# Kernel tuning notes

Hardware: AMD Instinct MI355X
Metric: run time of the kernel (lower is better)

## Reference

```python
import jax, jax.numpy as jnp
import numpy as np

N_NODES = 50000
ELU_ALPHA = 0.2  # torch.nn.ELU(0.2): alpha=0.2


def _elu(v, alpha):
    return jnp.where(v > 0, v, alpha * jnp.expm1(v))


def setup_inputs() -> dict:
    key = jax.random.key(0)
    k1, k2, k3, k4, k5 = jax.random.split(key, 5)
    fin, H, F = 128, 4, 32
    E = 1600000
    return {
        "x": jax.random.normal(k1, (N_NODES, fin), dtype=jnp.float32),
        "W": jax.random.normal(k2, (fin, H * F), dtype=jnp.float32) * (1.414 / np.sqrt(fin)),
        "a_src": jax.random.normal(k3, (H, F), dtype=jnp.float32) * 0.1,
        "a_tgt": jax.random.normal(k4, (H, F), dtype=jnp.float32) * 0.1,
        "edge_index": jax.random.randint(k5, (E, 2), 0, N_NODES, dtype=jnp.int64),
    }


def reference(x, W, a_src, a_tgt, edge_index):
    # GAT layer (dropout omitted: eval mode). x: [N, fin]
    N = x.shape[0]
    H, F = a_src.shape
    xp = (x @ W).reshape(N, H, F)                 # projected node feats [N,H,F]
    s_src = jnp.einsum("nhf,hf->nh", xp, a_src)   # per-head source scores [N,H]
    s_tgt = jnp.einsum("nhf,hf->nh", xp, a_tgt)   # per-head target scores [N,H]

    src = edge_index[:, 0]
    tgt = edge_index[:, 1]

    # edge-wise gather (the memory-bound hotspot)
    e = _elu(s_src[src] + s_tgt[tgt], ELU_ALPHA)  # [E,H]

    # segment softmax over edges sharing a target node
    m = jax.ops.segment_max(e, tgt, num_segments=N)           # [N,H]
    m = jnp.where(jnp.isfinite(m), m, 0.0)
    ex = jnp.exp(e - m[tgt])                                  # [E,H]
    denom = jax.ops.segment_sum(ex, tgt, num_segments=N)      # [N,H]
    alpha = ex / denom[tgt]                                   # [E,H]

    # gather source features, weight, scatter-add into target nodes
    msg = alpha[:, :, None] * xp[src]                          # [E,H,F]
    out = jax.ops.segment_sum(msg, tgt, num_segments=N)        # [N,H,F]
    return out.reshape(N, H * F)                               # concat heads
```

## Files before the change

### kernel.cpp

```cpp
#include <hip/hip_runtime.h>
#include <hip/hip_bf16.h>
#include <math.h>

#define FIN 128
#define NHEAD 4
#define CH 128
#define ELU_A 0.2f

#define BSHIFT 8
#define NB 196
#define CAP 16384
#define T_EDGES 2048

typedef unsigned int uint32;
typedef __attribute__((ext_vector_type(8))) short short8;
typedef __attribute__((ext_vector_type(4))) float f32x4;

__device__ __forceinline__ float bf16lo(uint32 u) {
    union { uint32 i; float f; } c; c.i = u << 16; return c.f;
}
__device__ __forceinline__ float bf16hi(uint32 u) {
    union { uint32 i; float f; } c; c.i = u & 0xffff0000u; return c.f;
}
__device__ __forceinline__ unsigned short f2b(float f) {
    union { float f; uint32 u; } c; c.f = f;
    uint32 u = c.u;
    return (unsigned short)((u + 0x7fffu + ((u >> 16) & 1u)) >> 16);
}

union SMem {
    struct {
        uint32 stage[T_EDGES];
        int hist[256], scanbuf[256], loff[256], cnt2[256], base[256];
    } p;
    unsigned short wt[128][136];
    unsigned short cbuf[4][16][132];
};

__global__ __launch_bounds__(256) void mega_kernel(
    const int2* __restrict__ ei2, int* __restrict__ bcnt,
    uint32* __restrict__ ebuck, const float* __restrict__ x,
    const float* __restrict__ W, unsigned short* __restrict__ xpb,
    const float* __restrict__ a_src, const float* __restrict__ a_tgt,
    float* __restrict__ s_src, float* __restrict__ s_tgt,
    int E, int N, int PB)
{
    __shared__ SMem sm;
    const int tid = threadIdx.x;

    if ((int)blockIdx.x < PB) {
        const int e0 = blockIdx.x * T_EDGES;
        const int tile = min(T_EDGES, E - e0);

        sm.p.hist[tid] = 0; sm.p.cnt2[tid] = 0;
        __syncthreads();

        uint32 rec[8];
#pragma unroll
        for (int j = 0; j < 8; ++j) {
            int idx = e0 + j * 256 + tid;
            if (idx < E) {
                int2 p = ei2[idx];
                rec[j] = (uint32)p.x | ((uint32)p.y << 16);
                atomicAdd(&sm.p.hist[p.y >> BSHIFT], 1);
            } else rec[j] = 0xFFFFFFFFu;
        }
        __syncthreads();

        sm.p.scanbuf[tid] = sm.p.hist[tid];
        __syncthreads();
        for (int off = 1; off < 256; off <<= 1) {
            int v = (tid >= off) ? sm.p.scanbuf[tid - off] : 0;
            __syncthreads();
            sm.p.scanbuf[tid] += v;
            __syncthreads();
        }
        sm.p.loff[tid] = sm.p.scanbuf[tid] - sm.p.hist[tid];
        if (tid < NB && sm.p.hist[tid] > 0)
            sm.p.base[tid] = tid * CAP + atomicAdd(&bcnt[tid], sm.p.hist[tid]);
        __syncthreads();

#pragma unroll
        for (int j = 0; j < 8; ++j) {
            if (rec[j] != 0xFFFFFFFFu) {
                int b = rec[j] >> (16 + BSHIFT);
                int r = atomicAdd(&sm.p.cnt2[b], 1);
                sm.p.stage[sm.p.loff[b] + r] = rec[j];
            }
        }
        __syncthreads();

        for (int i = tid; i < tile; i += 256) {
            uint32 rc = sm.p.stage[i];
            int b = rc >> (16 + BSHIFT);
            ebuck[(size_t)sm.p.base[b] + (i - sm.p.loff[b])] = rc;
        }
        return;
    }

    const int gb = blockIdx.x - PB;

    for (int i = tid; i < FIN * CH / 2; i += 256) {
        int n  = i & 127;
        int k2 = i >> 7;
        float w0 = W[(size_t)(2 * k2 + 0) * CH + n];
        float w1 = W[(size_t)(2 * k2 + 1) * CH + n];
        uint32 pk = (uint32)f2b(w0) | ((uint32)f2b(w1) << 16);
        *(uint32*)&sm.wt[n][2 * k2] = pk;
    }
    __syncthreads();

    const int lane = tid & 63;
    const int wid  = tid >> 6;
    const int rowbase = gb * 64 + wid * 16;

    const int rr   = min(rowbase + (lane & 15), N - 1);
    const int krow = (lane >> 4) * 8;

    f32x4 acc[8];
#pragma unroll
    for (int c = 0; c < 8; ++c) acc[c] = (f32x4){0.f, 0.f, 0.f, 0.f};

#pragma unroll
    for (int s = 0; s < 4; ++s) {
        const int koff = s * 32 + krow;
        const float* xr = x + (size_t)rr * FIN + koff;
        float4 p0 = *(const float4*)xr;
        float4 p1 = *(const float4*)(xr + 4);
        short8 af;
        af[0] = (short)f2b(p0.x); af[1] = (short)f2b(p0.y);
        af[2] = (short)f2b(p0.z); af[3] = (short)f2b(p0.w);
        af[4] = (short)f2b(p1.x); af[5] = (short)f2b(p1.y);
        af[6] = (short)f2b(p1.z); af[7] = (short)f2b(p1.w);
#pragma unroll
        for (int c = 0; c < 8; ++c) {
            const short8 bf = *(const short8*)&sm.wt[c * 16 + (lane & 15)][koff];
            acc[c] = __builtin_amdgcn_mfma_f32_16x16x32_bf16(af, bf, acc[c], 0, 0, 0);
        }
    }
    __syncthreads();

#pragma unroll
    for (int c = 0; c < 8; ++c)
#pragma unroll
        for (int r = 0; r < 4; ++r)
            sm.cbuf[wid][(lane >> 4) * 4 + r][c * 16 + (lane & 15)] = f2b(acc[c][r]);
    __syncthreads();

    for (int r = 0; r < 16; ++r) {
        int row = rowbase + r;
        if (row < N) {
            uint32 v = *(const uint32*)&sm.cbuf[wid][r][lane * 2];
            *(uint32*)&xpb[(size_t)row * CH + lane * 2] = v;
        }
    }

    {
        const int srow = lane >> 2;
        const int sh   = lane & 3;
        const unsigned short* cp = &sm.cbuf[wid][srow][sh * 32];
        const float* as = a_src + sh * 32;
        const float* at = a_tgt + sh * 32;
        float ps = 0.f, pt = 0.f;
#pragma unroll
        for (int q = 0; q < 4; ++q) {
            uint4 u = *(const uint4*)&cp[q * 8];
            float4 a0 = *(const float4*)&as[q * 8];
            float4 a1 = *(const float4*)&as[q * 8 + 4];
            float4 b0 = *(const float4*)&at[q * 8];
            float4 b1 = *(const float4*)&at[q * 8 + 4];
            float l0 = bf16lo(u.x), h0 = bf16hi(u.x);
            float l1 = bf16lo(u.y), h1 = bf16hi(u.y);
            float l2 = bf16lo(u.z), h2 = bf16hi(u.z);
            float l3 = bf16lo(u.w), h3 = bf16hi(u.w);
            ps += l0*a0.x + h0*a0.y + l1*a0.z + h1*a0.w
                + l2*a1.x + h2*a1.y + l3*a1.z + h3*a1.w;
            pt += l0*b0.x + h0*b0.y + l1*b0.z + h1*b0.w
                + l2*b1.x + h2*b1.y + l3*b1.z + h3*b1.w;
        }
        int node = rowbase + srow;
        if (node < N) {
            s_src[(size_t)node * NHEAD + sh] = ps;
            s_tgt[(size_t)node * NHEAD + sh] = pt;
        }
    }
}

__global__ __launch_bounds__(1024) void fine_scatter_kernel(
    const uint32* __restrict__ ebuck, const int* __restrict__ bcnt,
    int* __restrict__ deg, int* __restrict__ rowptr,
    int* __restrict__ srcs, int N)
{
    __shared__ int ldeg[256], psum[256], lcur[256], red[256];
    const int b = blockIdx.x;
    const int tid = threadIdx.x;

    if (tid < 256) {
        red[tid]  = (tid < b) ? bcnt[tid] : 0;
        ldeg[tid] = 0;
    }
    __syncthreads();
    for (int off = 128; off >= 1; off >>= 1) {
        if (tid < off) red[tid] += red[tid + off];
        __syncthreads();
    }
    const int gb = red[0];

    const int cnt = bcnt[b];
    const uint32* rp = ebuck + (size_t)b * CAP;

    for (int i = tid; i < cnt; i += 1024)
        atomicAdd(&ldeg[(rp[i] >> 16) & 255], 1);
    __syncthreads();

    if (tid < 256) psum[tid] = ldeg[tid];
    __syncthreads();
    for (int off = 1; off < 256; off <<= 1) {
        int u = 0;
        if (tid < 256 && tid >= off) u = psum[tid - off];
        __syncthreads();
        if (tid < 256) psum[tid] += u;
        __syncthreads();
    }

    if (tid < 256) {
        int pref = gb + psum[tid] - ldeg[tid];
        lcur[tid] = pref;
        int node = b * 256 + tid;
        if (node < N) { deg[node] = ldeg[tid]; rowptr[node] = pref; }
    }
    __syncthreads();

    for (int i = tid; i < cnt; i += 1024) {
        uint32 rc = rp[i];
        int pos = atomicAdd(&lcur[(rc >> 16) & 255], 1);
        srcs[pos] = rc & 0xffff;
    }
}

__global__ __launch_bounds__(256) void aggregate_kernel(
    const int* __restrict__ srcs, const int* __restrict__ rowptr,
    const int* __restrict__ deg, const float* __restrict__ s_src,
    const float* __restrict__ s_tgt, const uint32* __restrict__ xpb,
    float* __restrict__ out, int N)
{
    const int lane = threadIdx.x & 63;
    const int wid  = __builtin_amdgcn_readfirstlane(threadIdx.x >> 6);
    const int t = blockIdx.x * 4 + wid;
    if (t >= N) return;

    const int start = __builtin_amdgcn_readfirstlane(rowptr[t]);
    const int d     = __builtin_amdgcn_readfirstlane(deg[t]);
    const int h     = lane >> 4;
    const float st_h = s_tgt[(size_t)t * NHEAD + h];

    float accx = 0.0f, accy = 0.0f, dsum = 0.0f;
    int k = 0;

#define ACC(E, X) { dsum += (E); accx += (E) * bf16lo(X); accy += (E) * bf16hi(X); }

    const int cj16 = lane & 15;
    const int bb16 = h * 16;
    for (; k + 16 <= d; k += 16) {
        int   sv = srcs[start + k + cj16];
        float a  = s_src[(size_t)sv * NHEAD + h];
        float v  = a + st_h;
        float u  = v > 0.0f ? v : ELU_A * (__expf(v) - 1.0f);
        float e  = __expf(u);

        int s0 = srcs[start + k + 0],  s1 = srcs[start + k + 1];
        int s2 = srcs[start + k + 2],  s3 = srcs[start + k + 3];
        int s4 = srcs[start + k + 4],  s5 = srcs[start + k + 5];
        int s6 = srcs[start + k + 6],  s7 = srcs[start + k + 7];
        int s8 = srcs[start + k + 8],  s9 = srcs[start + k + 9];
        int sa = srcs[start + k + 10], sb = srcs[start + k + 11];
        int sc = srcs[start + k + 12], sd = srcs[start + k + 13];
        int se = srcs[start + k + 14], sf = srcs[start + k + 15];

        uint32 x0 = xpb[(size_t)s0 * 64 + lane], x1 = xpb[(size_t)s1 * 64 + lane];
        uint32 x2 = xpb[(size_t)s2 * 64 + lane], x3 = xpb[(size_t)s3 * 64 + lane];
        uint32 x4 = xpb[(size_t)s4 * 64 + lane], x5 = xpb[(size_t)s5 * 64 + lane];
        uint32 x6 = xpb[(size_t)s6 * 64 + lane], x7 = xpb[(size_t)s7 * 64 + lane];
        uint32 x8 = xpb[(size_t)s8 * 64 + lane], x9 = xpb[(size_t)s9 * 64 + lane];
        uint32 xa = xpb[(size_t)sa * 64 + lane], xb = xpb[(size_t)sb * 64 + lane];
        uint32 xc = xpb[(size_t)sc * 64 + lane], xd = xpb[(size_t)sd * 64 + lane];
        uint32 xe = xpb[(size_t)se * 64 + lane], xf = xpb[(size_t)sf * 64 + lane];

        float e0 = __shfl(e, bb16 + 0),  e1 = __shfl(e, bb16 + 1);
        float e2 = __shfl(e, bb16 + 2),  e3 = __shfl(e, bb16 + 3);
        float e4 = __shfl(e, bb16 + 4),  e5 = __shfl(e, bb16 + 5);
        float e6 = __shfl(e, bb16 + 6),  e7 = __shfl(e, bb16 + 7);
        float e8 = __shfl(e, bb16 + 8),  e9 = __shfl(e, bb16 + 9);
        float ea = __shfl(e, bb16 + 10), eb = __shfl(e, bb16 + 11);
        float ec = __shfl(e, bb16 + 12), ed = __shfl(e, bb16 + 13);
        float ee = __shfl(e, bb16 + 14), ef = __shfl(e, bb16 + 15);

        ACC(e0, x0) ACC(e1, x1) ACC(e2, x2) ACC(e3, x3)
        ACC(e4, x4) ACC(e5, x5) ACC(e6, x6) ACC(e7, x7)
        ACC(e8, x8) ACC(e9, x9) ACC(ea, xa) ACC(eb, xb)
        ACC(ec, xc) ACC(ed, xd) ACC(ee, xe) ACC(ef, xf)
    }

    const int cj8 = lane & 7;
    const int chh = (lane >> 3) & 3;
    const float st_c = s_tgt[(size_t)t * NHEAD + chh];
    const int bb8 = h * 8;
    for (; k + 8 <= d; k += 8) {
        int   sv = srcs[start + k + cj8];
        float a  = s_src[(size_t)sv * NHEAD + chh];
        float v  = a + st_c;
        float u  = v > 0.0f ? v : ELU_A * (__expf(v) - 1.0f);
        float e  = __expf(u);

        int s0 = srcs[start + k + 0], s1 = srcs[start + k + 1];
        int s2 = srcs[start + k + 2], s3 = srcs[start + k + 3];
        int s4 = srcs[start + k + 4], s5 = srcs[start + k + 5];
        int s6 = srcs[start + k + 6], s7 = srcs[start + k + 7];

        uint32 x0 = xpb[(size_t)s0 * 64 + lane], x1 = xpb[(size_t)s1 * 64 + lane];
        uint32 x2 = xpb[(size_t)s2 * 64 + lane], x3 = xpb[(size_t)s3 * 64 + lane];
        uint32 x4 = xpb[(size_t)s4 * 64 + lane], x5 = xpb[(size_t)s5 * 64 + lane];
        uint32 x6 = xpb[(size_t)s6 * 64 + lane], x7 = xpb[(size_t)s7 * 64 + lane];

        float e0 = __shfl(e, bb8 + 0), e1 = __shfl(e, bb8 + 1);
        float e2 = __shfl(e, bb8 + 2), e3 = __shfl(e, bb8 + 3);
        float e4 = __shfl(e, bb8 + 4), e5 = __shfl(e, bb8 + 5);
        float e6 = __shfl(e, bb8 + 6), e7 = __shfl(e, bb8 + 7);

        ACC(e0, x0) ACC(e1, x1) ACC(e2, x2) ACC(e3, x3)
        ACC(e4, x4) ACC(e5, x5) ACC(e6, x6) ACC(e7, x7)
    }

    for (; k < d; ++k) {
        int   s  = srcs[start + k];
        float a  = s_src[(size_t)s * NHEAD + h];
        uint32 xv = xpb[(size_t)s * 64 + lane];
        float v = a + st_h;
        float u = v > 0.0f ? v : ELU_A * (__expf(v) - 1.0f);
        float e = __expf(u);
        ACC(e, xv)
    }
#undef ACC

    float inv = (d > 0) ? 1.0f / dsum : 0.0f;
    float2 o = make_float2(accx * inv, accy * inv);
    *(float2*)&out[(size_t)t * CH + lane * 2] = o;
}

extern "C" void kernel_launch(void* const* d_in, const int* in_sizes, int n_in,
                              void* d_out, int out_size, void* d_ws, size_t ws_size,
                              hipStream_t stream)
{
    const float* x     = (const float*)d_in[0];
    const float* W     = (const float*)d_in[1];
    const float* a_src = (const float*)d_in[2];
    const float* a_tgt = (const float*)d_in[3];
    const int*   ei    = (const int*)d_in[4];

    const int N = in_sizes[0] / FIN;
    const int E = in_sizes[4] / 2;
    const int PB = (E + T_EDGES - 1) / T_EDGES;
    const int GB = (N + 63) / 64;

    char* ws = (char*)d_ws;
    unsigned short* xpb = (unsigned short*)ws;  ws += (size_t)N * CH * sizeof(unsigned short);
    float* s_src  = (float*)ws;                 ws += (size_t)N * NHEAD * sizeof(float);
    float* s_tgt  = (float*)ws;                 ws += (size_t)N * NHEAD * sizeof(float);
    int*   deg    = (int*)ws;                   ws += (size_t)N * sizeof(int);
    int*   bcnt   = (int*)ws;                   ws += (size_t)NB * sizeof(int);
    int*   rowptr = (int*)ws;                   ws += (size_t)N * sizeof(int);
    int*   srcs   = (int*)ws;                   ws += (size_t)E * sizeof(int);
    uint32* ebuck = (uint32*)ws;                ws += (size_t)NB * CAP * sizeof(uint32);

    float* out = (float*)d_out;
    const int2* ei2 = (const int2*)ei;

    hipMemsetAsync(bcnt, 0, (size_t)NB * sizeof(int), stream);

    mega_kernel<<<PB + GB, 256, 0, stream>>>(
        ei2, bcnt, ebuck, x, W, xpb, a_src, a_tgt, s_src, s_tgt, E, N, PB);
    fine_scatter_kernel<<<NB, 1024, 0, stream>>>(
        ebuck, bcnt, deg, rowptr, srcs, N);
    aggregate_kernel<<<(N + 3) / 4, 256, 0, stream>>>(
        srcs, rowptr, deg, s_src, s_tgt, (const uint32*)xpb, out, N);
}
```

Before: 120.5 us.

## Fuse fine scatter into aggregation with per-block CSR held in LDS

Merges the fine-scatter and aggregate kernels into one. Each of four blocks per coarse bucket rescans the bucket, builds degree and prefix for its 64 nodes, and places source indices in shared memory; its waves then aggregate 8 nodes each. This removes the global deg/rowptr/srcs round trip and one launch. In exchange each bucket is read four times, each wave walks its nodes serially with fewer waves in flight, and a fixed LDS capacity silently drops edges when a 64-node group has too many.

After: 142.7 us. 18.4% more time.

```diff
diff --git a/kernel.cpp b/kernel.cpp
--- a/kernel.cpp
+++ b/kernel.cpp
@@ -11,6 +11,7 @@
 #define NB 196
 #define CAP 16384
 #define T_EDGES 2048
+#define LCAP 2944
 
 typedef unsigned int uint32;
 typedef __attribute__((ext_vector_type(8))) short short8;
@@ -186,165 +187,158 @@
     }
 }
 
-__global__ __launch_bounds__(1024) void fine_scatter_kernel(
+__global__ __launch_bounds__(512) void scatter_aggregate_kernel(
     const uint32* __restrict__ ebuck, const int* __restrict__ bcnt,
-    int* __restrict__ deg, int* __restrict__ rowptr,
-    int* __restrict__ srcs, int N)
+    const float* __restrict__ s_src, const float* __restrict__ s_tgt,
+    const uint32* __restrict__ xpb, float* __restrict__ out, int N)
 {
-    __shared__ int ldeg[256], psum[256], lcur[256], red[256];
-    const int b = blockIdx.x;
+    __shared__ int lsrcs[LCAP];
+    __shared__ int ldeg[64], psum[64], lcur[64];
+    const int B   = blockIdx.x >> 2;
+    const int q   = blockIdx.x & 3;
     const int tid = threadIdx.x;
-
-    if (tid < 256) {
-        red[tid]  = (tid < b) ? bcnt[tid] : 0;
-        ldeg[tid] = 0;
-    }
-    __syncthreads();
-    for (int off = 128; off >= 1; off >>= 1) {
-        if (tid < off) red[tid] += red[tid + off];
-        __syncthreads();
-    }
-    const int gb = red[0];
-
-    const int cnt = bcnt[b];
-    const uint32* rp = ebuck + (size_t)b * CAP;
-
-    for (int i = tid; i < cnt; i += 1024)
-        atomicAdd(&ldeg[(rp[i] >> 16) & 255], 1);
-    __syncthreads();
-
-    if (tid < 256) psum[tid] = ldeg[tid];
-    __syncthreads();
-    for (int off = 1; off < 256; off <<= 1) {
+    const int node0 = B * 256 + q * 64;
+
+    if (tid < 64) ldeg[tid] = 0;
+    __syncthreads();
+
+    const int cnt = bcnt[B];
+    const uint32* rp = ebuck + (size_t)B * CAP;
+
+    for (int i = tid; i < cnt; i += 512) {
+        uint32 rc = rp[i];
+        int local = (rc >> 16) & 255;
+        if ((local >> 6) == q) atomicAdd(&ldeg[local & 63], 1);
+    }
+    __syncthreads();
+
+    if (tid < 64) psum[tid] = ldeg[tid];
+    __syncthreads();
+    for (int off = 1; off < 64; off <<= 1) {
         int u = 0;
-        if (tid < 256 && tid >= off) u = psum[tid - off];
-        __syncthreads();
-        if (tid < 256) psum[tid] += u;
-        __syncthreads();
-    }
-
-    if (tid < 256) {
-        int pref = gb + psum[tid] - ldeg[tid];
-        lcur[tid] = pref;
-        int node = b * 256 + tid;
-        if (node < N) { deg[node] = ldeg[tid]; rowptr[node] = pref; }
-    }
-    __syncthreads();
-
-    for (int i = tid; i < cnt; i += 1024) {
+        if (tid < 64 && tid >= off) u = psum[tid - off];
+        __syncthreads();
+        if (tid < 64) psum[tid] += u;
+        __syncthreads();
+    }
+    if (tid < 64) lcur[tid] = psum[tid] - ldeg[tid];
+    __syncthreads();
+
+    for (int i = tid; i < cnt; i += 512) {
         uint32 rc = rp[i];
-        int pos = atomicAdd(&lcur[(rc >> 16) & 255], 1);
-        srcs[pos] = rc & 0xffff;
-    }
-}
-
-__global__ __launch_bounds__(256) void aggregate_kernel(
-    const int* __restrict__ srcs, const int* __restrict__ rowptr,
-    const int* __restrict__ deg, const float* __restrict__ s_src,
-    const float* __restrict__ s_tgt, const uint32* __restrict__ xpb,
-    float* __restrict__ out, int N)
-{
-    const int lane = threadIdx.x & 63;
-    const int wid  = __builtin_amdgcn_readfirstlane(threadIdx.x >> 6);
-    const int t = blockIdx.x * 4 + wid;
-    if (t >= N) return;
-
-    const int start = __builtin_amdgcn_readfirstlane(rowptr[t]);
-    const int d     = __builtin_amdgcn_readfirstlane(deg[t]);
-    const int h     = lane >> 4;
-    const float st_h = s_tgt[(size_t)t * NHEAD + h];
-
-    float accx = 0.0f, accy = 0.0f, dsum = 0.0f;
-    int k = 0;
+        int local = (rc >> 16) & 255;
+        if ((local >> 6) == q) {
+            int pos = atomicAdd(&lcur[local & 63], 1);
+            if (pos < LCAP) lsrcs[pos] = (int)(rc & 0xffff);
+        }
+    }
+    __syncthreads();
+
+    const int lane = tid & 63;
+    const int wid  = tid >> 6;
+    const int h    = lane >> 4;
 
 #define ACC(E, X) { dsum += (E); accx += (E) * bf16lo(X); accy += (E) * bf16hi(X); }
 
-    const int cj16 = lane & 15;
-    const int bb16 = h * 16;
-    for (; k + 16 <= d; k += 16) {
-        int   sv = srcs[start + k + cj16];
-        float a  = s_src[(size_t)sv * NHEAD + h];
-        float v  = a + st_h;
-        float u  = v > 0.0f ? v : ELU_A * (__expf(v) - 1.0f);
-        float e  = __expf(u);
-
-        int s0 = srcs[start + k + 0],  s1 = srcs[start + k + 1];
-        int s2 = srcs[start + k + 2],  s3 = srcs[start + k + 3];
-        int s4 = srcs[start + k + 4],  s5 = srcs[start + k + 5];
-        int s6 = srcs[start + k + 6],  s7 = srcs[start + k + 7];
-        int s8 = srcs[start + k + 8],  s9 = srcs[start + k + 9];
-        int sa = srcs[start + k + 10], sb = srcs[start + k + 11];
-        int sc = srcs[start + k + 12], sd = srcs[start + k + 13];
-        int se = srcs[start + k + 14], sf = srcs[start + k + 15];
-
-        uint32 x0 = xpb[(size_t)s0 * 64 + lane], x1 = xpb[(size_t)s1 * 64 + lane];
-        uint32 x2 = xpb[(size_t)s2 * 64 + lane], x3 = xpb[(size_t)s3 * 64 + lane];
-        uint32 x4 = xpb[(size_t)s4 * 64 + lane], x5 = xpb[(size_t)s5 * 64 + lane];
-        uint32 x6 = xpb[(size_t)s6 * 64 + lane], x7 = xpb[(size_t)s7 * 64 + lane];
-        uint32 x8 = xpb[(size_t)s8 * 64 + lane], x9 = xpb[(size_t)s9 * 64 + lane];
-        uint32 xa = xpb[(size_t)sa * 64 + lane], xb = xpb[(size_t)sb * 64 + lane];
-        uint32 xc = xpb[(size_t)sc * 64 + lane], xd = xpb[(size_t)sd * 64 + lane];
-        uint32 xe = xpb[(size_t)se * 64 + lane], xf = xpb[(size_t)sf * 64 + lane];
-
-        float e0 = __shfl(e, bb16 + 0),  e1 = __shfl(e, bb16 + 1);
-        float e2 = __shfl(e, bb16 + 2),  e3 = __shfl(e, bb16 + 3);
-        float e4 = __shfl(e, bb16 + 4),  e5 = __shfl(e, bb16 + 5);
-        float e6 = __shfl(e, bb16 + 6),  e7 = __shfl(e, bb16 + 7);
-        float e8 = __shfl(e, bb16 + 8),  e9 = __shfl(e, bb16 + 9);
-        float ea = __shfl(e, bb16 + 10), eb = __shfl(e, bb16 + 11);
-        float ec = __shfl(e, bb16 + 12), ed = __shfl(e, bb16 + 13);
-        float ee = __shfl(e, bb16 + 14), ef = __shfl(e, bb16 + 15);
-
-        ACC(e0, x0) ACC(e1, x1) ACC(e2, x2) ACC(e3, x3)
-        ACC(e4, x4) ACC(e5, x5) ACC(e6, x6) ACC(e7, x7)
-        ACC(e8, x8) ACC(e9, x9) ACC(ea, xa) ACC(eb, xb)
-        ACC(ec, xc) ACC(ed, xd) ACC(ee, xe) ACC(ef, xf)
-    }
-
-    const int cj8 = lane & 7;
-    const int chh = (lane >> 3) & 3;
-    const float st_c = s_tgt[(size_t)t * NHEAD + chh];
-    const int bb8 = h * 8;
-    for (; k + 8 <= d; k += 8) {
-        int   sv = srcs[start + k + cj8];
-        float a  = s_src[(size_t)sv * NHEAD + chh];
-        float v  = a + st_c;
-        float u  = v > 0.0f ? v : ELU_A * (__expf(v) - 1.0f);
-        float e  = __expf(u);
-
-        int s0 = srcs[start + k + 0], s1 = srcs[start + k + 1];
-        int s2 = srcs[start + k + 2], s3 = srcs[start + k + 3];
-        int s4 = srcs[start + k + 4], s5 = srcs[start + k + 5];
-        int s6 = srcs[start + k + 6], s7 = srcs[start + k + 7];
-
-        uint32 x0 = xpb[(size_t)s0 * 64 + lane], x1 = xpb[(size_t)s1 * 64 + lane];
-        uint32 x2 = xpb[(size_t)s2 * 64 + lane], x3 = xpb[(size_t)s3 * 64 + lane];
-        uint32 x4 = xpb[(size_t)s4 * 64 + lane], x5 = xpb[(size_t)s5 * 64 + lane];
-        uint32 x6 = xpb[(size_t)s6 * 64 + lane], x7 = xpb[(size_t)s7 * 64 + lane];
-
-        float e0 = __shfl(e, bb8 + 0), e1 = __shfl(e, bb8 + 1);
-        float e2 = __shfl(e, bb8 + 2), e3 = __shfl(e, bb8 + 3);
-        float e4 = __shfl(e, bb8 + 4), e5 = __shfl(e, bb8 + 5);
-        float e6 = __shfl(e, bb8 + 6), e7 = __shfl(e, bb8 + 7);
-
-        ACC(e0, x0) ACC(e1, x1) ACC(e2, x2) ACC(e3, x3)
-        ACC(e4, x4) ACC(e5, x5) ACC(e6, x6) ACC(e7, x7)
-    }
-
-    for (; k < d; ++k) {
-        int   s  = srcs[start + k];
-        float a  = s_src[(size_t)s * NHEAD + h];
-        uint32 xv = xpb[(size_t)s * 64 + lane];
-        float v = a + st_h;
-        float u = v > 0.0f ? v : ELU_A * (__expf(v) - 1.0f);
-        float e = __expf(u);
-        ACC(e, xv)
+    for (int i = 0; i < 8; ++i) {
+        const int ln = wid * 8 + i;
+        const int t  = node0 + ln;
+        if (t >= N) continue;
+
+        const int d     = ldeg[ln];
+        const int start = psum[ln] - d;
+        const float st_h = s_tgt[(size_t)t * NHEAD + h];
+
+        float accx = 0.0f, accy = 0.0f, dsum = 0.0f;
+        int k = 0;
+
+        const int cj16 = lane & 15;
+        const int bb16 = h * 16;
+        for (; k + 16 <= d; k += 16) {
+            int   sv = lsrcs[start + k + cj16];
+            float a  = s_src[(size_t)sv * NHEAD + h];
+            float v  = a + st_h;
+            float u  = v > 0.0f ? v : ELU_A * (__expf(v) - 1.0f);
+            float e  = __expf(u);
+
+            int s0 = lsrcs[start + k + 0],  s1 = lsrcs[start + k + 1];
+            int s2 = lsrcs[start + k + 2],  s3 = lsrcs[start + k + 3];
+            int s4 = lsrcs[start + k + 4],  s5 = lsrcs[start + k + 5];
+            int s6 = lsrcs[start + k + 6],  s7 = lsrcs[start + k + 7];
+            int s8 = lsrcs[start + k + 8],  s9 = lsrcs[start + k + 9];
+            int sa = lsrcs[start + k + 10], sb = lsrcs[start + k + 11];
+            int sc = lsrcs[start + k + 12], sd = lsrcs[start + k + 13];
+            int se = lsrcs[start + k + 14], sf = lsrcs[start + k + 15];
+
+            uint32 x0 = xpb[(size_t)s0 * 64 + lane], x1 = xpb[(size_t)s1 * 64 + lane];
+            uint32 x2 = xpb[(size_t)s2 * 64 + lane], x3 = xpb[(size_t)s3 * 64 + lane];
+            uint32 x4 = xpb[(size_t)s4 * 64 + lane], x5 = xpb[(size_t)s5 * 64 + lane];
+            uint32 x6 = xpb[(size_t)s6 * 64 + lane], x7 = xpb[(size_t)s7 * 64 + lane];
+            uint32 x8 = xpb[(size_t)s8 * 64 + lane], x9 = xpb[(size_t)s9 * 64 + lane];
+            uint32 xa = xpb[(size_t)sa * 64 + lane], xb = xpb[(size_t)sb * 64 + lane];
+            uint32 xc = xpb[(size_t)sc * 64 + lane], xd = xpb[(size_t)sd * 64 + lane];
+            uint32 xe = xpb[(size_t)se * 64 + lane], xf = xpb[(size_t)sf * 64 + lane];
+
+            float e0 = __shfl(e, bb16 + 0),  e1 = __shfl(e, bb16 + 1);
+            float e2 = __shfl(e, bb16 + 2),  e3 = __shfl(e, bb16 + 3);
+            float e4 = __shfl(e, bb16 + 4),  e5 = __shfl(e, bb16 + 5);
+            float e6 = __shfl(e, bb16 + 6),  e7 = __shfl(e, bb16 + 7);
+            float e8 = __shfl(e, bb16 + 8),  e9 = __shfl(e, bb16 + 9);
+            float ea = __shfl(e, bb16 + 10), eb = __shfl(e, bb16 + 11);
+            float ec = __shfl(e, bb16 + 12), ed = __shfl(e, bb16 + 13);
+            float ee = __shfl(e, bb16 + 14), ef = __shfl(e, bb16 + 15);
+
+            ACC(e0, x0) ACC(e1, x1) ACC(e2, x2) ACC(e3, x3)
+            ACC(e4, x4) ACC(e5, x5) ACC(e6, x6) ACC(e7, x7)
+            ACC(e8, x8) ACC(e9, x9) ACC(ea, xa) ACC(eb, xb)
+            ACC(ec, xc) ACC(ed, xd) ACC(ee, xe) ACC(ef, xf)
+        }
+
+        const int cj8 = lane & 7;
+        const int chh = (lane >> 3) & 3;
+        const float st_c = s_tgt[(size_t)t * NHEAD + chh];
+        const int bb8 = h * 8;
+        for (; k + 8 <= d; k += 8) {
+            int   sv = lsrcs[start + k + cj8];
+            float a  = s_src[(size_t)sv * NHEAD + chh];
+            float v  = a + st_c;
+            float u  = v > 0.0f ? v : ELU_A * (__expf(v) - 1.0f);
+            float e  = __expf(u);
+
+            int s0 = lsrcs[start + k + 0], s1 = lsrcs[start + k + 1];
+            int s2 = lsrcs[start + k + 2], s3 = lsrcs[start + k + 3];
+            int s4 = lsrcs[start + k + 4], s5 = lsrcs[start + k + 5];
+            int s6 = lsrcs[start + k + 6], s7 = lsrcs[start + k + 7];
+
+            uint32 x0 = xpb[(size_t)s0 * 64 + lane], x1 = xpb[(size_t)s1 * 64 + lane];
+            uint32 x2 = xpb[(size_t)s2 * 64 + lane], x3 = xpb[(size_t)s3 * 64 + lane];
+            uint32 x4 = xpb[(size_t)s4 * 64 + lane], x5 = xpb[(size_t)s5 * 64 + lane];
+            uint32 x6 = xpb[(size_t)s6 * 64 + lane], x7 = xpb[(size_t)s7 * 64 + lane];
+
+            float e0 = __shfl(e, bb8 + 0), e1 = __shfl(e, bb8 + 1);
+            float e2 = __shfl(e, bb8 + 2), e3 = __shfl(e, bb8 + 3);
+            float e4 = __shfl(e, bb8 + 4), e5 = __shfl(e, bb8 + 5);
+            float e6 = __shfl(e, bb8 + 6), e7 = __shfl(e, bb8 + 7);
+
+            ACC(e0, x0) ACC(e1, x1) ACC(e2, x2) ACC(e3, x3)
+            ACC(e4, x4) ACC(e5, x5) ACC(e6, x6) ACC(e7, x7)
+        }
+
+        for (; k < d; ++k) {
+            int   s  = lsrcs[start + k];
+            float a  = s_src[(size_t)s * NHEAD + h];
+            uint32 xv = xpb[(size_t)s * 64 + lane];
+            float v = a + st_h;
+            float u = v > 0.0f ? v : ELU_A * (__expf(v) - 1.0f);
+            float e = __expf(u);
+            ACC(e, xv)
+        }
+
+        float inv = (d > 0) ? 1.0f / dsum : 0.0f;
+        float2 o = make_float2(accx * inv, accy * inv);
+        *(float2*)&out[(size_t)t * CH + lane * 2] = o;
     }
 #undef ACC
-
-    float inv = (d > 0) ? 1.0f / dsum : 0.0f;
-    float2 o = make_float2(accx * inv, accy * inv);
-    *(float2*)&out[(size_t)t * CH + lane * 2] = o;
 }
 
 extern "C" void kernel_launch(void* const* d_in, const int* in_sizes, int n_in,
@@ -366,10 +360,7 @@
     unsigned short* xpb = (unsigned short*)ws;  ws += (size_t)N * CH * sizeof(unsigned short);
     float* s_src  = (float*)ws;                 ws += (size_t)N * NHEAD * sizeof(float);
     float* s_tgt  = (float*)ws;                 ws += (size_t)N * NHEAD * sizeof(float);
-    int*   deg    = (int*)ws;                   ws += (size_t)N * sizeof(int);
     int*   bcnt   = (int*)ws;                   ws += (size_t)NB * sizeof(int);
-    int*   rowptr = (int*)ws;                   ws += (size_t)N * sizeof(int);
-    int*   srcs   = (int*)ws;                   ws += (size_t)E * sizeof(int);
     uint32* ebuck = (uint32*)ws;                ws += (size_t)NB * CAP * sizeof(uint32);
 
     float* out = (float*)d_out;
@@ -379,8 +370,6 @@
 
     mega_kernel<<<PB + GB, 256, 0, stream>>>(
         ei2, bcnt, ebuck, x, W, xpb, a_src, a_tgt, s_src, s_tgt, E, N, PB);
-    fine_scatter_kernel<<<NB, 1024, 0, stream>>>(
-        ebuck, bcnt, deg, rowptr, srcs, N);
-    aggregate_kernel<<<(N + 3) / 4, 256, 0, stream>>>(
-        srcs, rowptr, deg, s_src, s_tgt, (const uint32*)xpb, out, N);
-}
+    scatter_aggregate_kernel<<<NB * 4, 512, 0, stream>>>(
+        ebuck, bcnt, s_src, s_tgt, (const uint32*)xpb, out, N);
+}
```
